# Optimization experiments

Measured on AMD Instinct MI355X. Metric: run time of the kernel, lower is better.

Reference implementation:

```python
import jax, jax.numpy as jnp
import numpy as np

B, D, H, W, C = 1, 6, 128, 128, 180
NH = 6
HD = C // NH
SCALE = HD ** -0.5
WS = (2, 8, 8)
SS = (1, 4, 4)
N = WS[0] * WS[1] * WS[2]  # 128 tokens per 3D window
HID = int(C * 2.0)  # GEGLU hidden = 360


def _rel_pos_index(ws):
    d, h, w = np.meshgrid(np.arange(ws[0]), np.arange(ws[1]), np.arange(ws[2]), indexing='ij')
    coords = np.stack([d, h, w]).reshape(3, -1)  # (3, N)
    rel = (coords[:, :, None] - coords[:, None, :]).transpose(1, 2, 0).astype(np.int64)
    rel[:, :, 0] += ws[0] - 1
    rel[:, :, 1] += ws[1] - 1
    rel[:, :, 2] += ws[2] - 1
    rel[:, :, 0] *= (2 * ws[1] - 1) * (2 * ws[2] - 1)
    rel[:, :, 1] *= (2 * ws[2] - 1)
    return rel.sum(-1).astype(np.int32)  # (N, N)


def _sine_pos(hw, nf, temperature=10000.0):
    scale = 2.0 * np.pi
    ones = np.ones((1, hw[0], hw[1]), np.float64)
    y = np.cumsum(ones, 1)
    x = np.cumsum(ones, 2)
    eps = 1e-6
    y = y / (y[:, -1:, :] + eps) * scale
    x = x / (x[:, :, -1:] + eps) * scale
    dim_t = temperature ** (2 * (np.arange(nf) // 2) / nf)
    px = x[..., None] / dim_t
    py = y[..., None] / dim_t
    px = np.stack([np.sin(px[..., 0::2]), np.cos(px[..., 1::2])], -1).reshape(1, hw[0], hw[1], -1)
    py = np.stack([np.sin(py[..., 0::2]), np.cos(py[..., 1::2])], -1).reshape(1, hw[0], hw[1], -1)
    pos = np.concatenate([py, px], -1)  # (1, H, W, 2*nf)
    return pos.reshape(1, hw[0] * hw[1], -1).astype(np.float32)


def _compute_mask():
    img = np.zeros((1, D, H, W, 1), np.float32)
    cnt = 0
    sl = lambda w, s: (slice(0, -w), slice(-w, -s), slice(-s, None))
    for ds in sl(WS[0], SS[0]):
        for hs in sl(WS[1], SS[1]):
            for ws_ in sl(WS[2], SS[2]):
                img[:, ds, hs, ws_, :] = cnt
                cnt += 1
    mw = img.reshape(1, D // WS[0], WS[0], H // WS[1], WS[1], W // WS[2], WS[2], 1)
    mw = mw.transpose(0, 1, 3, 5, 2, 4, 6, 7).reshape(-1, N)
    am = mw[:, None, :] - mw[:, :, None]
    return np.where(am != 0, -100.0, 0.0).astype(np.float32)  # (nW, N, N)


def win_part(x):
    b = x.shape[0]
    x = x.reshape(b, D // WS[0], WS[0], H // WS[1], WS[1], W // WS[2], WS[2], C)
    return x.transpose(0, 1, 3, 5, 2, 4, 6, 7).reshape(-1, N, C)


def win_rev(w, b):
    x = w.reshape(b, D // WS[0], H // WS[1], W // WS[2], WS[0], WS[1], WS[2], C)
    return x.transpose(0, 1, 4, 2, 5, 3, 6, 7).reshape(b, D, H, W, C)


def ln(x, g, b):
    m = x.mean(-1, keepdims=True)
    v = ((x - m) ** 2).mean(-1, keepdims=True)
    return (x - m) / jnp.sqrt(v + 1e-5) * g + b


def attn_fn(q, k, v, bias, mask):
    # q,k,v: (B_, NH, n, HD); bias: (NH, n, n) or None; mask: (nW, n, n) or None
    a = jnp.einsum('bhnd,bhmd->bhnm', q * SCALE, k)
    if bias is not None:
        a = a + bias[None]
    if mask is not None:
        nW = mask.shape[0]
        a = a.reshape(-1, nW, NH, a.shape[-2], a.shape[-1]) + mask[None, :, None]
        a = a.reshape(-1, NH, a.shape[-2], a.shape[-1])
    a = jax.nn.softmax(a, axis=-1)
    o = jnp.einsum('bhnm,bhmd->bhnd', a, v)
    return o.transpose(0, 2, 1, 3).reshape(o.shape[0], o.shape[2], -1)


def setup_inputs() -> dict:
    key = jax.random.key(0)
    ks = jax.random.split(key, 9)
    p = lambda k, shape: jax.random.normal(k, shape, jnp.float32) * 0.02
    return {
        'x': jax.random.normal(ks[0], (B, D, H, W, C), jnp.float32),
        'mask': jnp.asarray(_compute_mask()),
        'g1': jnp.ones((C,), jnp.float32), 'b1': jnp.zeros((C,), jnp.float32),
        'g2': jnp.ones((C,), jnp.float32), 'b2': jnp.zeros((C,), jnp.float32),
        'w_qkv_self': p(ks[1], (C, 3 * C)), 'b_qkv_self': jnp.zeros((3 * C,), jnp.float32),
        'w_qkv_mut': p(ks[2], (C, 3 * C)), 'b_qkv_mut': jnp.zeros((3 * C,), jnp.float32),
        'rpb_table': p(ks[3], ((2 * WS[0] - 1) * (2 * WS[1] - 1) * (2 * WS[2] - 1), NH)),
        'pos_bias': jnp.asarray(_sine_pos((WS[1], WS[2]), C // 2)),
        'w_proj': p(ks[4], (2 * C, C)), 'b_proj': jnp.zeros((C,), jnp.float32),
        'w_fc11': p(ks[5], (C, HID)), 'b_fc11': jnp.zeros((HID,), jnp.float32),
        'w_fc12': p(ks[6], (C, HID)), 'b_fc12': jnp.zeros((HID,), jnp.float32),
        'w_fc2': p(ks[7], (HID, C)), 'b_fc2': jnp.zeros((C,), jnp.float32),
        'rpi': jnp.asarray(_rel_pos_index(WS)),
    }


def reference(x, mask, g1, b1, g2, b2, w_qkv_self, b_qkv_self, w_qkv_mut, b_qkv_mut,
              rpb_table, pos_bias, w_proj, b_proj, w_fc11, b_fc11, w_fc12, b_fc12,
              w_fc2, b_fc2, rpi):
    # --- attention branch ---
    h = ln(x, g1, b1)
    h = jnp.roll(h, (-SS[0], -SS[1], -SS[2]), axis=(1, 2, 3))  # cyclic shift
    xw = win_part(h)  # (B*nW, N, C)
    B_ = xw.shape[0]

    def qkv(xin, wq, bq):
        t = (xin @ wq + bq).reshape(B_, -1, 3, NH, HD).transpose(2, 0, 3, 1, 4)
        return t[0], t[1], t[2]

    q, k, v = qkv(xw, w_qkv_self, b_qkv_self)
    bias = rpb_table[rpi.reshape(-1)].reshape(N, N, NH).transpose(2, 0, 1)
    x_self = attn_fn(q, k, v, bias, mask)

    # mutual attention between the two frames of each window
    pb = jnp.concatenate([pos_bias, pos_bias], axis=1)  # (1, N, C)
    qm, km, vm = qkv(xw + pb, w_qkv_mut, b_qkv_mut)
    half = N // 2
    q1, q2 = qm[:, :, :half], qm[:, :, half:]
    k1, k2 = km[:, :, :half], km[:, :, half:]
    v1, v2 = vm[:, :, :half], vm[:, :, half:]
    m2 = mask[:, :half, :half]
    x1 = attn_fn(q2, k1, v1, None, m2)
    x2 = attn_fn(q1, k2, v2, None, m2)
    xo = jnp.concatenate([jnp.concatenate([x1, x2], axis=1), x_self], axis=2)  # (B_, N, 2C)
    xo = xo @ w_proj + b_proj
    out = win_rev(xo, x.shape[0])
    out = jnp.roll(out, (SS[0], SS[1], SS[2]), axis=(1, 2, 3))
    x = x + out

    # --- GEGLU MLP branch ---
    h = ln(x, g2, b2)
    h = jax.nn.gelu(h @ w_fc11 + b_fc11, approximate=False) * (h @ w_fc12 + b_fc12)
    x = x + (h @ w_fc2 + b_fc2)
    return x
```

## Files before the change

### kernel.cpp

```cpp
#include <hip/hip_runtime.h>
#include <hip/hip_bf16.h>
#include <math.h>
#include <cstdio>


typedef __hip_bfloat16 bf16;
typedef __attribute__((ext_vector_type(8))) short short8;
typedef __attribute__((ext_vector_type(4))) unsigned short us4;
typedef __attribute__((ext_vector_type(4))) float f32x4;

#define SCALE_F 0.18257418583505536f
#define SZPE 18874368u

__device__ __forceinline__ bf16  f2b(float v){ return __float2bfloat16(v); }
__device__ __forceinline__ float bu2f(unsigned short u){
    union { unsigned int i; float f; } x; x.i = ((unsigned int)u) << 16; return x.f;
}
__device__ __forceinline__ f32x4 mfma16(short8 a, short8 b, f32x4 c){
    return __builtin_amdgcn_mfma_f32_16x16x32_bf16(a, b, c, 0, 0, 0);
}

__device__ __forceinline__ void gld16(const bf16* g, bf16* s){
    __builtin_amdgcn_global_load_lds(
        (const __attribute__((address_space(1))) unsigned int*)g,
        (__attribute__((address_space(3))) unsigned int*)s, 16, 0, 0);
}

__device__ __forceinline__ float gelu_erf(float x){
    float z  = fabsf(x) * 0.70710678118654752f;
    float t  = __builtin_amdgcn_rcpf(fmaf(0.3275911f, z, 1.f));
    float p  = fmaf(fmaf(fmaf(fmaf(1.061405429f, t, -1.453152027f),
                              t, 1.421413741f), t, -0.284496736f), t, 0.254829592f) * t;
    float e  = __expf(-z * z);
    float er = fmaf(-p, e, 1.f);
    er = (x >= 0.f) ? er : -er;
    return 0.5f * x * (1.f + er);
}

__device__ __forceinline__ int xswz(){
    return (blockIdx.x & 7) * ((int)gridDim.x >> 3) + ((int)blockIdx.x >> 3);
}

__device__ __forceinline__ int wincnt(int win, int tok){
    int d = (win >> 8) * 2 + (tok >> 6);
    int h = ((win >> 4) & 15) * 8 + ((tok >> 3) & 7);
    int w = (win & 15) * 8 + (tok & 7);
    int rd = (d >= 4) + (d >= 5);
    int rh = (h >= 120) + (h >= 124);
    int rw = (w >= 120) + (w >= 124);
    return (rd * 3 + rh) * 3 + rw;
}

__device__ __forceinline__ size_t wrev_base(int row){
    int win = row >> 7, tok = row & 127;
    int wd = win >> 8, wh = (win >> 4) & 15, ww = win & 15;
    int td = tok >> 6, th = (tok >> 3) & 7, tw = tok & 7;
    int d = wd * 2 + td + 1; if (d >= 6) d -= 6;
    int h = (wh * 8 + th + 4) & 127;
    int wcol = (ww * 8 + tw + 4) & 127;
    return ((size_t)((d * 128 + h) * 128 + wcol)) * 180;
}

__global__ __launch_bounds__(256) void k_pack_qkv(const float* __restrict__ w,
                                                  const float* __restrict__ bias,
                                                  bf16* __restrict__ Bt,
                                                  float* __restrict__ bb)
{
    int idx = blockIdx.x * 256 + threadIdx.x;
    int n = idx / 192, k = idx - n * 192;
    int three = n / 192;
    int rem = n - three * 192, nh = rem >> 5, hdp = rem & 31;
    int srcc = three * 180 + nh * 30 + hdp;
    float v = 0.f;
    if (hdp < 30 && k < 180) v = w[(size_t)k * 540 + srcc];
    if (three == 0) v *= SCALE_F;
    Bt[(size_t)n * 192 + k] = f2b(v);
    if (k == 0) bb[n] = (hdp < 30) ? ((three == 0 ? SCALE_F : 1.f) * bias[srcc]) : 0.f;
}

__global__ __launch_bounds__(256) void k_pack(const float* __restrict__ w,
                                              int NW, int K, int KP,
                                              bf16* __restrict__ Bt)
{
    int idx = blockIdx.x * 256 + threadIdx.x;
    int n = idx / KP, k = idx - n * KP;
    float v = (n < NW && k < K) ? w[(size_t)k * NW + n] : 0.f;
    Bt[idx] = f2b(v);
}

__global__ __launch_bounds__(256) void k_rpbg(const float* __restrict__ rpb,
                                              const int* __restrict__ rpi,
                                              bf16* __restrict__ biasrT)
{
    int n = blockIdx.x * 256 + threadIdx.x;
    int nh = n >> 14, rc = n & 16383;
    int row = rc >> 7, col = rc & 127;
    biasrT[((size_t)nh * 128 + col) * 128 + row] = f2b(rpb[rpi[rc] * 6 + nh]);
}

__global__ __launch_bounds__(256) void k_zpad(bf16* __restrict__ attn)
{
    int gi = blockIdx.x * 256 + threadIdx.x;
    int row = gi / 3, part = gi - row * 3;
    *(uint4*)&attn[(size_t)row * 384 + 360 + part * 8] = make_uint4(0u,0u,0u,0u);
}

template<bool ROLL_PB>
__global__ __launch_bounds__(256) void k_ln(const float* __restrict__ x,
                                            const float* __restrict__ g,
                                            const float* __restrict__ b,
                                            const float* __restrict__ pb,
                                            bf16* __restrict__ xw,
                                            bf16* __restrict__ xwm)
{
    int row  = blockIdx.x * 4 + (threadIdx.x >> 6);
    int lane = threadIdx.x & 63;
    const float* src;
    if (ROLL_PB) {
        src = x + wrev_base(row) - 0;
    } else {
        src = x + (size_t)row * 180;
    }
    float v0 = src[lane];
    float v1 = src[lane + 64];
    float v2 = (lane < 52) ? src[lane + 128] : 0.f;
    float s  = v0 + v1 + v2;
    float ss = v0*v0 + v1*v1 + v2*v2;
    #pragma unroll
    for (int o = 32; o > 0; o >>= 1) { s += __shfl_xor(s, o, 64); ss += __shfl_xor(ss, o, 64); }
    float mean = s * (1.f/180.f);
    float var  = ss * (1.f/180.f) - mean*mean;
    float rstd = rsqrtf(var + 1e-5f);

    bf16* dst = xw + (size_t)row * 192;
    float y0 = (v0-mean)*rstd*g[lane]     + b[lane];
    float y1 = (v1-mean)*rstd*g[lane+64]  + b[lane+64];
    float y2 = (lane < 52) ? ((v2-mean)*rstd*g[lane+128] + b[lane+128]) : 0.f;
    dst[lane]      = f2b(y0);
    dst[lane+64]   = f2b(y1);
    if (lane < 52) dst[lane+128] = f2b(y2);
    if (lane < 12) dst[180+lane] = f2b(0.f);
    if (ROLL_PB) {
        const float* pbr = pb + (size_t)(row & 63) * 180;
        bf16* dm = xwm + (size_t)row * 192;
        dm[lane]      = f2b(y0 + pbr[lane]);
        dm[lane+64]   = f2b(y1 + pbr[lane+64]);
        if (lane < 52) dm[lane+128] = f2b(y2 + pbr[lane+128]);
        if (lane < 12) dm[180+lane] = f2b(0.f);
    }
}

template<int KP, bool DUAL>
__device__ __forceinline__ void mm2(const bf16* __restrict__ A,
                                    const bf16* __restrict__ Bt1,
                                    const bf16* __restrict__ Bt2,
                                    bf16* As, bf16* Bs1, bf16* Bs2,
                                    int m0, int n0,
                                    f32x4 (&acc1)[2][4], f32x4 (&acc2)[2][4])
{
    const int tid = threadIdx.x;
    const int w = tid >> 6, l = tid & 63, q = l >> 4, c = l & 15;
    const int lr = l >> 3, lj = l & 7;
    const int swz = ((lj ^ lr) << 3);
    #pragma unroll
    for (int ks = 0; ks < KP / 64; ks++) {
        #pragma unroll
        for (int e = 0; e < 4; e++) {
            int m = (e * 4 + w) * 8 + lr;
            gld16(&A[(size_t)(m0 + m) * KP + ks * 64 + swz], &As[((e * 4 + w) * 8) * 64]);
        }
        #pragma unroll
        for (int e = 0; e < 2; e++) {
            int n = (e * 4 + w) * 8 + lr;
            gld16(&Bt1[(size_t)(n0 + n) * KP + ks * 64 + swz], &Bs1[((e * 4 + w) * 8) * 64]);
            if (DUAL)
                gld16(&Bt2[(size_t)(n0 + n) * KP + ks * 64 + swz], &Bs2[((e * 4 + w) * 8) * 64]);
        }
        __syncthreads();
        #pragma unroll
        for (int k32 = 0; k32 < 2; k32++) {
            int koff = (((k32 * 4 + q) ^ (c & 7)) << 3);
            short8 a[2];
            #pragma unroll
            for (int mt = 0; mt < 2; mt++)
                a[mt] = *(const short8*)&As[(w * 32 + mt * 16 + c) * 64 + koff];
            #pragma unroll
            for (int nt = 0; nt < 4; nt++) {
                short8 b1 = *(const short8*)&Bs1[(nt * 16 + c) * 64 + koff];
                #pragma unroll
                for (int mt = 0; mt < 2; mt++) acc1[mt][nt] = mfma16(a[mt], b1, acc1[mt][nt]);
                if (DUAL) {
                    short8 b2 = *(const short8*)&Bs2[(nt * 16 + c) * 64 + koff];
                    #pragma unroll
                    for (int mt = 0; mt < 2; mt++) acc2[mt][nt] = mfma16(a[mt], b2, acc2[mt][nt]);
                }
            }
        }
        __syncthreads();
    }
}

__device__ __forceinline__ int cs_idx(int row, int colt){
    return row * 64 + ((((colt >> 3) ^ ((row >> 2) & 7)) << 3) | (colt & 7));
}

__global__ __launch_bounds__(256) void k_qkv(const bf16* __restrict__ A,
                                             const bf16* __restrict__ Bt,
                                             const float* __restrict__ bb,
                                             bf16* __restrict__ outq)
{
    __shared__ __align__(16) bf16 As[128 * 64];
    __shared__ __align__(16) bf16 Bs[64 * 64];
    int bid = xswz();
    int n0 = (bid % 9) * 64, m0 = (bid / 9) * 128;
    f32x4 a1[2][4] = {}, a2[2][4];
    mm2<192, false>(A, Bt, nullptr, As, Bs, nullptr, m0, n0, a1, a2);

    int tid = threadIdx.x, w = tid >> 6, l = tid & 63, q = l >> 4, c = l & 15;
    bf16* Cs = As;
    #pragma unroll
    for (int mt = 0; mt < 2; mt++)
      #pragma unroll
      for (int nt = 0; nt < 4; nt++)
        #pragma unroll
        for (int r = 0; r < 4; r++) {
            int row = w * 32 + mt * 16 + q * 4 + r;
            int colt = nt * 16 + c;
            Cs[cs_idx(row, colt)] = f2b(a1[mt][nt][r] + bb[n0 + colt]);
        }
    __syncthreads();
    int win = m0 >> 7;
    #pragma unroll
    for (int e = 0; e < 4; e++) {
        int gi = e * 256 + tid;
        int row = gi >> 3, j = gi & 7, c8 = j * 8;
        int col = n0 + c8;
        int three = col / 192, rem = col - three * 192;
        int nh = rem >> 5, hdp = rem & 31;
        bf16* dst = outq + (size_t)three * SZPE + ((size_t)(win * 6 + nh) * 128 + row) * 32 + hdp;
        *(uint4*)dst = *(const uint4*)&Cs[row * 64 + ((j ^ ((row >> 2) & 7)) << 3)];
    }
}

__global__ __launch_bounds__(256) void k_proj(const bf16* __restrict__ A,
                                              const bf16* __restrict__ Bt,
                                              const float* __restrict__ bias,
                                              const float* __restrict__ xin,
                                              float* __restrict__ res)
{
    __shared__ __align__(16) char smem[24576];
    bf16*  As = (bf16*)smem;
    bf16*  Bs = (bf16*)(smem + 16384);
    float* Cs = (float*)smem;
    int bid = xswz();
    int n0 = (bid % 3) * 64, m0 = (bid / 3) * 128;
    f32x4 a1[2][4] = {}, a2[2][4];
    mm2<384, false>(A, Bt, nullptr, As, Bs, nullptr, m0, n0, a1, a2);

    int tid = threadIdx.x, w = tid >> 6, l = tid & 63, q = l >> 4, c = l & 15;
    #pragma unroll
    for (int h = 0; h < 2; h++) {
        __syncthreads();
        if ((w >> 1) == h) {
            #pragma unroll
            for (int mt = 0; mt < 2; mt++)
              #pragma unroll
              for (int nt = 0; nt < 4; nt++)
                #pragma unroll
                for (int r = 0; r < 4; r++) {
                    int rl = (w & 1) * 32 + mt * 16 + q * 4 + r;
                    Cs[rl * 76 + nt * 16 + c] = a1[mt][nt][r];
                }
        }
        __syncthreads();
        #pragma unroll
        for (int e = 0; e < 4; e++) {
            int slot = e * 256 + tid;
            int rl = slot >> 4, cq = slot & 15;
            int col = n0 + cq * 4;
            if (col < 180) {
                size_t base = wrev_base(m0 + h * 64 + rl) + col;
                float4 xi = *(const float4*)&xin[base];
                float4 bi = *(const float4*)&bias[col];
                const float* cp = &Cs[rl * 76 + cq * 4];
                float4 o;
                o.x = xi.x + cp[0] + bi.x;
                o.y = xi.y + cp[1] + bi.y;
                o.z = xi.z + cp[2] + bi.z;
                o.w = xi.w + cp[3] + bi.w;
                *(float4*)&res[base] = o;
            }
        }
    }
}

__global__ __launch_bounds__(256) void k_fc1(const bf16* __restrict__ A,
                                             const bf16* __restrict__ Bt1,
                                             const float* __restrict__ bb1,
                                             const bf16* __restrict__ Bt2,
                                             const float* __restrict__ bb2,
                                             bf16* __restrict__ hid)
{
    __shared__ __align__(16) bf16 As[128 * 64];
    __shared__ __align__(16) bf16 Bs1[64 * 64];
    __shared__ __align__(16) bf16 Bs2[64 * 64];
    int bid = xswz();
    int n0 = (bid % 6) * 64, m0 = (bid / 6) * 128;
    f32x4 a1[2][4] = {}, a2[2][4] = {};
    mm2<192, true>(A, Bt1, Bt2, As, Bs1, Bs2, m0, n0, a1, a2);

    int tid = threadIdx.x, w = tid >> 6, l = tid & 63, q = l >> 4, c = l & 15;
    bf16* Cs = As;
    #pragma unroll
    for (int mt = 0; mt < 2; mt++)
      #pragma unroll
      for (int nt = 0; nt < 4; nt++)
        #pragma unroll
        for (int r = 0; r < 4; r++) {
            int row = w * 32 + mt * 16 + q * 4 + r;
            int colt = nt * 16 + c;
            int col = n0 + colt;
            float hv = 0.f;
            if (col < 360)
                hv = gelu_erf(a1[mt][nt][r] + bb1[col]) * (a2[mt][nt][r] + bb2[col]);
            Cs[cs_idx(row, colt)] = f2b(hv);
        }
    __syncthreads();
    #pragma unroll
    for (int e = 0; e < 4; e++) {
        int gi = e * 256 + tid;
        int row = gi >> 3, j = gi & 7, c8 = j * 8;
        *(uint4*)&hid[(size_t)(m0 + row) * 384 + n0 + c8] =
            *(const uint4*)&Cs[row * 64 + ((j ^ ((row >> 2) & 7)) << 3)];
    }
}

__global__ __launch_bounds__(256) void k_fc2(const bf16* __restrict__ A,
                                             const bf16* __restrict__ Bt,
                                             const float* __restrict__ bias,
                                             float* __restrict__ out)
{
    __shared__ __align__(16) char smem[24576];
    bf16*  As = (bf16*)smem;
    bf16*  Bs = (bf16*)(smem + 16384);
    float* Cs = (float*)smem;
    int bid = xswz();
    int n0 = (bid % 3) * 64, m0 = (bid / 3) * 128;
    f32x4 a1[2][4] = {}, a2[2][4];
    mm2<384, false>(A, Bt, nullptr, As, Bs, nullptr, m0, n0, a1, a2);

    int tid = threadIdx.x, w = tid >> 6, l = tid & 63, q = l >> 4, c = l & 15;
    #pragma unroll
    for (int h = 0; h < 2; h++) {
        __syncthreads();
        if ((w >> 1) == h) {
            #pragma unroll
            for (int mt = 0; mt < 2; mt++)
              #pragma unroll
              for (int nt = 0; nt < 4; nt++)
                #pragma unroll
                for (int r = 0; r < 4; r++) {
                    int rl = (w & 1) * 32 + mt * 16 + q * 4 + r;
                    Cs[rl * 76 + nt * 16 + c] = a1[mt][nt][r];
                }
        }
        __syncthreads();
        #pragma unroll
        for (int e = 0; e < 4; e++) {
            int slot = e * 256 + tid;
            int rl = slot >> 4, cq = slot & 15;
            int col = n0 + cq * 4;
            if (col < 180) {
                size_t idx = (size_t)(m0 + h * 64 + rl) * 180 + col;
                float4 ov = *(const float4*)&out[idx];
                float4 bi = *(const float4*)&bias[col];
                const float* cp = &Cs[rl * 76 + cq * 4];
                ov.x += cp[0] + bi.x;
                ov.y += cp[1] + bi.y;
                ov.z += cp[2] + bi.z;
                ov.w += cp[3] + bi.w;
                *(float4*)&out[idx] = ov;
            }
        }
    }
}

template<bool MUT>
__global__ __launch_bounds__(256) void k_attn(const bf16* __restrict__ qkv,
                                              const bf16* __restrict__ biasrT,
                                              bf16* __restrict__ aout)
{
    __shared__ __align__(16) bf16 Vts[32 * 136];
    __shared__ __align__(16) bf16 Ps[128 * 136];

    int wh = blockIdx.x, win = wh / 6, nh = wh - win * 6;
    const bf16* qg = qkv + (size_t)wh * 4096;
    const bf16* kg = qg + (size_t)SZPE;
    const bf16* vg = qg + 2 * (size_t)SZPE;
    int tid = threadIdx.x, w = tid >> 6, l = tid & 63, q = l >> 4, c = l & 15;

    #pragma unroll
    for (int e = 0; e < 2; e++) {
        int base = (e * 256 + tid) * 8;
        int tok = base >> 5, hd0 = base & 31;
        uint4 vv = *(const uint4*)&vg[base];
        const bf16* pv = (const bf16*)&vv;
        #pragma unroll
        for (int i = 0; i < 8; i++) {
            int hd = hd0 + i;
            Vts[hd * 136 + (tok ^ (((hd >> 3) & 3) << 3))] = pv[i];
        }
    }

    f32x4 S[2][8];
    #pragma unroll
    for (int mt = 0; mt < 2; mt++)
        #pragma unroll
        for (int nt = 0; nt < 8; nt++) S[mt][nt] = (f32x4){0.f, 0.f, 0.f, 0.f};
    {
        short8 a[2];
        #pragma unroll
        for (int mt = 0; mt < 2; mt++) {
            int rq = w * 32 + mt * 16 + c;
            if (MUT) rq ^= 64;
            a[mt] = *(const short8*)&qg[rq * 32 + q * 8];
        }
        #pragma unroll
        for (int nt = 0; nt < 8; nt++) {
            short8 b = *(const short8*)&kg[(nt * 16 + c) * 32 + q * 8];
            #pragma unroll
            for (int mt = 0; mt < 2; mt++) S[mt][nt] = mfma16(a[mt], b, S[mt][nt]);
        }
    }

    int rcnt[2][4], ccnt[8];
    #pragma unroll
    for (int mt = 0; mt < 2; mt++)
        #pragma unroll
        for (int r = 0; r < 4; r++) {
            int row = w * 32 + mt * 16 + q * 4 + r;
            rcnt[mt][r] = wincnt(win, MUT ? (row & 63) : row);
        }
    #pragma unroll
    for (int nt = 0; nt < 8; nt++) {
        int col = nt * 16 + c;
        ccnt[nt] = wincnt(win, MUT ? (col & 63) : col);
    }

    float mx[2][4];
    #pragma unroll
    for (int mt = 0; mt < 2; mt++)
      #pragma unroll
      for (int r = 0; r < 4; r++) mx[mt][r] = -3.0e38f;

    #pragma unroll
    for (int mt = 0; mt < 2; mt++)
      #pragma unroll
      for (int nt = 0; nt < 8; nt++) {
        float bv[4];
        if (!MUT) {
            int col = nt * 16 + c;
            us4 bb = *(const us4*)&biasrT[((size_t)(nh * 128 + col)) * 128
                                          + w * 32 + mt * 16 + q * 4];
            #pragma unroll
            for (int r = 0; r < 4; r++) bv[r] = bu2f(bb[r]);
        }
        bool valid = (w < 2) == (nt < 4);
        #pragma unroll
        for (int r = 0; r < 4; r++) {
            float s = S[mt][nt][r];
            if (MUT) {
                s = (rcnt[mt][r] == ccnt[nt]) ? s : s - 100.f;
                s = valid ? s : -30000.f;
            } else {
                s += bv[r];
                if (rcnt[mt][r] != ccnt[nt]) s -= 100.f;
            }
            S[mt][nt][r] = s;
            mx[mt][r] = fmaxf(mx[mt][r], s);
        }
      }
    #pragma unroll
    for (int mt = 0; mt < 2; mt++)
      #pragma unroll
      for (int r = 0; r < 4; r++) {
          float m = mx[mt][r];
          #pragma unroll
          for (int o = 1; o < 16; o <<= 1) m = fmaxf(m, __shfl_xor(m, o, 64));
          mx[mt][r] = m;
      }

    float sm[2][4] = {};
    #pragma unroll
    for (int mt = 0; mt < 2; mt++)
      #pragma unroll
      for (int nt = 0; nt < 8; nt++)
        #pragma unroll
        for (int r = 0; r < 4; r++) {
            float p = __expf(S[mt][nt][r] - mx[mt][r]);
            sm[mt][r] += p;
            Ps[(w * 32 + mt * 16 + q * 4 + r) * 136 + ((nt * 16 + c) ^ (q << 3))] = f2b(p);
        }
    #pragma unroll
    for (int mt = 0; mt < 2; mt++)
      #pragma unroll
      for (int r = 0; r < 4; r++) {
          float s = sm[mt][r];
          #pragma unroll
          for (int o = 1; o < 16; o <<= 1) s += __shfl_xor(s, o, 64);
          sm[mt][r] = s;
      }
    __syncthreads();

    f32x4 O[2][2];
    #pragma unroll
    for (int mt = 0; mt < 2; mt++)
        #pragma unroll
        for (int nt = 0; nt < 2; nt++) O[mt][nt] = (f32x4){0.f, 0.f, 0.f, 0.f};
    #pragma unroll
    for (int ks = 0; ks < 4; ks++) {
        short8 a[2];
        #pragma unroll
        for (int mt = 0; mt < 2; mt++) {
            int row = w * 32 + mt * 16 + c;
            int xr = ((c >> 2) & 3) << 3;
            a[mt] = *(const short8*)&Ps[row * 136 + (ks * 32 + ((q << 3) ^ xr))];
        }
        #pragma unroll
        for (int nt = 0; nt < 2; nt++) {
            int hd = nt * 16 + c;
            int xv = ((hd >> 3) & 3) << 3;
            short8 b = *(const short8*)&Vts[hd * 136 + (ks * 32 + ((q << 3) ^ xv))];
            #pragma unroll
            for (int mt = 0; mt < 2; mt++) O[mt][nt] = mfma16(a[mt], b, O[mt][nt]);
        }
    }

    #pragma unroll
    for (int mt = 0; mt < 2; mt++)
      #pragma unroll
      for (int r = 0; r < 4; r++) {
          int row = w * 32 + mt * 16 + q * 4 + r;
          float inv = 1.f / sm[mt][r];
          #pragma unroll
          for (int nt = 0; nt < 2; nt++) {
              int col = nt * 16 + c;
              if (col < 30)
                  aout[((size_t)win * 128 + row) * 384 + (MUT ? 0 : 180) + nh * 30 + col] =
                      f2b(O[mt][nt][r] * inv);
          }
      }
}

extern "C" void kernel_launch(void* const* d_in, const int* in_sizes, int n_in,
                              void* d_out, int out_size, void* d_ws, size_t ws_size,
                              hipStream_t stream)
{
    const float* x     = (const float*)d_in[0];
    const float* mask  = (const float*)d_in[1];
    const float* g1    = (const float*)d_in[2];
    const float* b1    = (const float*)d_in[3];
    const float* g2    = (const float*)d_in[4];
    const float* b2    = (const float*)d_in[5];
    const float* wqs   = (const float*)d_in[6];
    const float* bqs   = (const float*)d_in[7];
    const float* wqm   = (const float*)d_in[8];
    const float* bqm   = (const float*)d_in[9];
    const float* rpb   = (const float*)d_in[10];
    const float* posb  = (const float*)d_in[11];
    const float* wproj = (const float*)d_in[12];
    const float* bproj = (const float*)d_in[13];
    const float* w11   = (const float*)d_in[14];
    const float* bf11  = (const float*)d_in[15];
    const float* w12   = (const float*)d_in[16];
    const float* bf12  = (const float*)d_in[17];
    const float* w2    = (const float*)d_in[18];
    const float* bf2   = (const float*)d_in[19];
    const int*   rpi   = (const int*)d_in[20];
    float* out = (float*)d_out;
    (void)mask;

    const size_t need = 265671168;
    if (ws_size < need) { fprintf(stderr, "[tmsa] ws too small: %zu < %zu\n", ws_size, need); return; }

    char* W = (char*)d_ws;
    bf16*  xw     = (bf16*)W;
    bf16*  xwm    = (bf16*)(W + 37748736);
    bf16*  attn   = (bf16*)(W + 75497472);
    bf16*  qkv    = (bf16*)(W + 150994944);
    bf16*  biasrT = (bf16*)(W + 264241152);
    bf16*  Btqs   = (bf16*)(W + 264634368);
    bf16*  Btqm   = (bf16*)(W + 264855552);
    float* bbqs   = (float*)(W + 265076736);
    float* bbqm   = (float*)(W + 265079040);
    bf16*  Btproj = (bf16*)(W + 265081344);
    bf16*  Btf11  = (bf16*)(W + 265228800);
    bf16*  Btf12  = (bf16*)(W + 265376256);
    bf16*  Btf2   = (bf16*)(W + 265523712);

    k_rpbg<<<dim3(384), 256, 0, stream>>>(rpb, rpi, biasrT);
    k_pack_qkv<<<dim3(432), 256, 0, stream>>>(wqs, bqs, Btqs, bbqs);
    k_pack_qkv<<<dim3(432), 256, 0, stream>>>(wqm, bqm, Btqm, bbqm);
    k_pack<<<dim3(288), 256, 0, stream>>>(wproj, 180, 360, 384, Btproj);
    k_pack<<<dim3(288), 256, 0, stream>>>(w11,   360, 180, 192, Btf11);
    k_pack<<<dim3(288), 256, 0, stream>>>(w12,   360, 180, 192, Btf12);
    k_pack<<<dim3(288), 256, 0, stream>>>(w2,    180, 360, 384, Btf2);

    k_ln<true><<<dim3(24576), 256, 0, stream>>>(x, g1, b1, posb, xw, xwm);
    k_zpad<<<dim3(1152), 256, 0, stream>>>(attn);
    k_qkv<<<dim3(6912), 256, 0, stream>>>(xw, Btqs, bbqs, qkv);
    k_attn<false><<<dim3(4608), 256, 0, stream>>>(qkv, biasrT, attn);
    k_qkv<<<dim3(6912), 256, 0, stream>>>(xwm, Btqm, bbqm, qkv);
    k_attn<true><<<dim3(4608), 256, 0, stream>>>(qkv, biasrT, attn);
    k_proj<<<dim3(2304), 256, 0, stream>>>(attn, Btproj, bproj, x, out);
    k_ln<false><<<dim3(24576), 256, 0, stream>>>(out, g2, b2, nullptr, xw, nullptr);
    k_fc1<<<dim3(4608), 256, 0, stream>>>(xw, Btf11, bf11, Btf12, bf12, attn);
    k_fc2<<<dim3(2304), 256, 0, stream>>>(attn, Btf2, bf2, out);
}
```

Measured before the change: 590.9 us.

## Merge setup kernels, vectorize layernorm, skip masked half in mutual attention

Seven weight-pack and bias-gather kernels plus the zero-pad kernel are merged into a single k_prep launch that dispatches on block index, cutting launch overhead. Layernorm now uses float4 loads and packed 4-wide bf16 stores instead of scalar accesses. Mutual attention computes only the 64 valid key columns per wave instead of all 128 with -30000 masking, halving its QK, softmax and PV work. These are three unrelated edits, and the block-index ranges in k_prep must exactly match the old grid sizes.

```diff
diff --git a/kernel.cpp b/kernel.cpp
--- a/kernel.cpp
+++ b/kernel.cpp
@@ -15,6 +15,13 @@
 __device__ __forceinline__ bf16  f2b(float v){ return __float2bfloat16(v); }
 __device__ __forceinline__ float bu2f(unsigned short u){
     union { unsigned int i; float f; } x; x.i = ((unsigned int)u) << 16; return x.f;
+}
+__device__ __forceinline__ us4 pack4(float a, float b, float c, float d){
+    us4 r;
+    bf16 t0 = f2b(a), t1 = f2b(b), t2 = f2b(c), t3 = f2b(d);
+    r[0] = *(unsigned short*)&t0; r[1] = *(unsigned short*)&t1;
+    r[2] = *(unsigned short*)&t2; r[3] = *(unsigned short*)&t3;
+    return r;
 }
 __device__ __forceinline__ f32x4 mfma16(short8 a, short8 b, f32x4 c){
     return __builtin_amdgcn_mfma_f32_16x16x32_bf16(a, b, c, 0, 0, 0);
@@ -61,12 +68,9 @@
     return ((size_t)((d * 128 + h) * 128 + wcol)) * 180;
 }
 
-__global__ __launch_bounds__(256) void k_pack_qkv(const float* __restrict__ w,
-                                                  const float* __restrict__ bias,
-                                                  bf16* __restrict__ Bt,
-                                                  float* __restrict__ bb)
-{
-    int idx = blockIdx.x * 256 + threadIdx.x;
+__device__ __forceinline__ void prep_pack_qkv(int idx, const float* w, const float* bias,
+                                              bf16* Bt, float* bb)
+{
     int n = idx / 192, k = idx - n * 192;
     int three = n / 192;
     int rem = n - three * 192, nh = rem >> 5, hdp = rem & 31;
@@ -77,32 +81,57 @@
     Bt[(size_t)n * 192 + k] = f2b(v);
     if (k == 0) bb[n] = (hdp < 30) ? ((three == 0 ? SCALE_F : 1.f) * bias[srcc]) : 0.f;
 }
-
-__global__ __launch_bounds__(256) void k_pack(const float* __restrict__ w,
-                                              int NW, int K, int KP,
-                                              bf16* __restrict__ Bt)
-{
-    int idx = blockIdx.x * 256 + threadIdx.x;
+__device__ __forceinline__ void prep_pack(int idx, const float* w,
+                                          int NW, int K, int KP, bf16* Bt)
+{
     int n = idx / KP, k = idx - n * KP;
     float v = (n < NW && k < K) ? w[(size_t)k * NW + n] : 0.f;
     Bt[idx] = f2b(v);
 }
-
-__global__ __launch_bounds__(256) void k_rpbg(const float* __restrict__ rpb,
+__global__ __launch_bounds__(256) void k_prep(const float* __restrict__ rpb,
                                               const int* __restrict__ rpi,
-                                              bf16* __restrict__ biasrT)
-{
-    int n = blockIdx.x * 256 + threadIdx.x;
-    int nh = n >> 14, rc = n & 16383;
-    int row = rc >> 7, col = rc & 127;
-    biasrT[((size_t)nh * 128 + col) * 128 + row] = f2b(rpb[rpi[rc] * 6 + nh]);
-}
-
-__global__ __launch_bounds__(256) void k_zpad(bf16* __restrict__ attn)
-{
-    int gi = blockIdx.x * 256 + threadIdx.x;
-    int row = gi / 3, part = gi - row * 3;
-    *(uint4*)&attn[(size_t)row * 384 + 360 + part * 8] = make_uint4(0u,0u,0u,0u);
+                                              bf16* __restrict__ biasrT,
+                                              const float* __restrict__ wqs,
+                                              const float* __restrict__ bqs,
+                                              bf16* __restrict__ Btqs,
+                                              float* __restrict__ bbqs,
+                                              const float* __restrict__ wqm,
+                                              const float* __restrict__ bqm,
+                                              bf16* __restrict__ Btqm,
+                                              float* __restrict__ bbqm,
+                                              const float* __restrict__ wproj,
+                                              bf16* __restrict__ Btproj,
+                                              const float* __restrict__ w11,
+                                              bf16* __restrict__ Btf11,
+                                              const float* __restrict__ w12,
+                                              bf16* __restrict__ Btf12,
+                                              const float* __restrict__ w2,
+                                              bf16* __restrict__ Btf2,
+                                              bf16* __restrict__ attn)
+{
+    int bid = blockIdx.x, tid = threadIdx.x;
+    if (bid < 384) {
+        int n = bid * 256 + tid;
+        int nh = n >> 14, rc = n & 16383;
+        int row = rc >> 7, col = rc & 127;
+        biasrT[((size_t)nh * 128 + col) * 128 + row] = f2b(rpb[rpi[rc] * 6 + nh]);
+    } else if (bid < 816) {
+        prep_pack_qkv((bid - 384) * 256 + tid, wqs, bqs, Btqs, bbqs);
+    } else if (bid < 1248) {
+        prep_pack_qkv((bid - 816) * 256 + tid, wqm, bqm, Btqm, bbqm);
+    } else if (bid < 1536) {
+        prep_pack((bid - 1248) * 256 + tid, wproj, 180, 360, 384, Btproj);
+    } else if (bid < 1824) {
+        prep_pack((bid - 1536) * 256 + tid, w11, 360, 180, 192, Btf11);
+    } else if (bid < 2112) {
+        prep_pack((bid - 1824) * 256 + tid, w12, 360, 180, 192, Btf12);
+    } else if (bid < 2400) {
+        prep_pack((bid - 2112) * 256 + tid, w2, 180, 360, 384, Btf2);
+    } else {
+        int gi = (bid - 2400) * 256 + tid;
+        int row = gi / 3, part = gi - row * 3;
+        *(uint4*)&attn[(size_t)row * 384 + 360 + part * 8] = make_uint4(0u,0u,0u,0u);
+    }
 }
 
 template<bool ROLL_PB>
@@ -115,17 +144,11 @@
 {
     int row  = blockIdx.x * 4 + (threadIdx.x >> 6);
     int lane = threadIdx.x & 63;
-    const float* src;
-    if (ROLL_PB) {
-        src = x + wrev_base(row) - 0;
-    } else {
-        src = x + (size_t)row * 180;
-    }
-    float v0 = src[lane];
-    float v1 = src[lane + 64];
-    float v2 = (lane < 52) ? src[lane + 128] : 0.f;
-    float s  = v0 + v1 + v2;
-    float ss = v0*v0 + v1*v1 + v2*v2;
+    const float* src = ROLL_PB ? (x + wrev_base(row)) : (x + (size_t)row * 180);
+    float4 v = make_float4(0.f, 0.f, 0.f, 0.f);
+    if (lane < 45) v = *(const float4*)&src[lane * 4];
+    float s  = v.x + v.y + v.z + v.w;
+    float ss = v.x*v.x + v.y*v.y + v.z*v.z + v.w*v.w;
     #pragma unroll
     for (int o = 32; o > 0; o >>= 1) { s += __shfl_xor(s, o, 64); ss += __shfl_xor(ss, o, 64); }
     float mean = s * (1.f/180.f);
@@ -133,20 +156,27 @@
     float rstd = rsqrtf(var + 1e-5f);
 
     bf16* dst = xw + (size_t)row * 192;
-    float y0 = (v0-mean)*rstd*g[lane]     + b[lane];
-    float y1 = (v1-mean)*rstd*g[lane+64]  + b[lane+64];
-    float y2 = (lane < 52) ? ((v2-mean)*rstd*g[lane+128] + b[lane+128]) : 0.f;
-    dst[lane]      = f2b(y0);
-    dst[lane+64]   = f2b(y1);
-    if (lane < 52) dst[lane+128] = f2b(y2);
-    if (lane < 12) dst[180+lane] = f2b(0.f);
+    float4 y = make_float4(0.f, 0.f, 0.f, 0.f);
+    if (lane < 45) {
+        float4 gv = *(const float4*)&g[lane * 4];
+        float4 bv = *(const float4*)&b[lane * 4];
+        y.x = (v.x - mean) * rstd * gv.x + bv.x;
+        y.y = (v.y - mean) * rstd * gv.y + bv.y;
+        y.z = (v.z - mean) * rstd * gv.z + bv.z;
+        y.w = (v.w - mean) * rstd * gv.w + bv.w;
+        *(us4*)&dst[lane * 4] = pack4(y.x, y.y, y.z, y.w);
+    } else if (lane < 48) {
+        *(us4*)&dst[lane * 4] = (us4){0, 0, 0, 0};
+    }
     if (ROLL_PB) {
-        const float* pbr = pb + (size_t)(row & 63) * 180;
         bf16* dm = xwm + (size_t)row * 192;
-        dm[lane]      = f2b(y0 + pbr[lane]);
-        dm[lane+64]   = f2b(y1 + pbr[lane+64]);
-        if (lane < 52) dm[lane+128] = f2b(y2 + pbr[lane+128]);
-        if (lane < 12) dm[180+lane] = f2b(0.f);
+        if (lane < 45) {
+            const float* pbr = pb + (size_t)(row & 63) * 180;
+            float4 pv = *(const float4*)&pbr[lane * 4];
+            *(us4*)&dm[lane * 4] = pack4(y.x + pv.x, y.y + pv.y, y.z + pv.z, y.w + pv.w);
+        } else if (lane < 48) {
+            *(us4*)&dm[lane * 4] = (us4){0, 0, 0, 0};
+        }
     }
 }
 
@@ -399,6 +429,9 @@
     const bf16* vg = qg + 2 * (size_t)SZPE;
     int tid = threadIdx.x, w = tid >> 6, l = tid & 63, q = l >> 4, c = l & 15;
 
+    constexpr int NT = MUT ? 4 : 8;
+    const int colbase = MUT ? ((w < 2) ? 0 : 64) : 0;
+
     #pragma unroll
     for (int e = 0; e < 2; e++) {
         int base = (e * 256 + tid) * 8;
@@ -412,11 +445,11 @@
         }
     }
 
-    f32x4 S[2][8];
-    #pragma unroll
-    for (int mt = 0; mt < 2; mt++)
-        #pragma unroll
-        for (int nt = 0; nt < 8; nt++) S[mt][nt] = (f32x4){0.f, 0.f, 0.f, 0.f};
+    f32x4 S[2][NT];
+    #pragma unroll
+    for (int mt = 0; mt < 2; mt++)
+        #pragma unroll
+        for (int nt = 0; nt < NT; nt++) S[mt][nt] = (f32x4){0.f, 0.f, 0.f, 0.f};
     {
         short8 a[2];
         #pragma unroll
@@ -426,14 +459,14 @@
             a[mt] = *(const short8*)&qg[rq * 32 + q * 8];
         }
         #pragma unroll
-        for (int nt = 0; nt < 8; nt++) {
-            short8 b = *(const short8*)&kg[(nt * 16 + c) * 32 + q * 8];
+        for (int nt = 0; nt < NT; nt++) {
+            short8 b = *(const short8*)&kg[(colbase + nt * 16 + c) * 32 + q * 8];
             #pragma unroll
             for (int mt = 0; mt < 2; mt++) S[mt][nt] = mfma16(a[mt], b, S[mt][nt]);
         }
     }
 
-    int rcnt[2][4], ccnt[8];
+    int rcnt[2][4], ccnt[NT];
     #pragma unroll
     for (int mt = 0; mt < 2; mt++)
         #pragma unroll
@@ -442,8 +475,8 @@
             rcnt[mt][r] = wincnt(win, MUT ? (row & 63) : row);
         }
     #pragma unroll
-    for (int nt = 0; nt < 8; nt++) {
-        int col = nt * 16 + c;
+    for (int nt = 0; nt < NT; nt++) {
+        int col = colbase + nt * 16 + c;
         ccnt[nt] = wincnt(win, MUT ? (col & 63) : col);
     }
 
@@ -456,7 +489,7 @@
     #pragma unroll
     for (int mt = 0; mt < 2; mt++)
       #pragma unroll
-      for (int nt = 0; nt < 8; nt++) {
+      for (int nt = 0; nt < NT; nt++) {
         float bv[4];
         if (!MUT) {
             int col = nt * 16 + c;
@@ -465,13 +498,11 @@
             #pragma unroll
             for (int r = 0; r < 4; r++) bv[r] = bu2f(bb[r]);
         }
-        bool valid = (w < 2) == (nt < 4);
         #pragma unroll
         for (int r = 0; r < 4; r++) {
             float s = S[mt][nt][r];
             if (MUT) {
                 s = (rcnt[mt][r] == ccnt[nt]) ? s : s - 100.f;
-                s = valid ? s : -30000.f;
             } else {
                 s += bv[r];
                 if (rcnt[mt][r] != ccnt[nt]) s -= 100.f;
@@ -494,12 +525,12 @@
     #pragma unroll
     for (int mt = 0; mt < 2; mt++)
       #pragma unroll
-      for (int nt = 0; nt < 8; nt++)
+      for (int nt = 0; nt < NT; nt++)
         #pragma unroll
         for (int r = 0; r < 4; r++) {
             float p = __expf(S[mt][nt][r] - mx[mt][r]);
             sm[mt][r] += p;
-            Ps[(w * 32 + mt * 16 + q * 4 + r) * 136 + ((nt * 16 + c) ^ (q << 3))] = f2b(p);
+            Ps[(w * 32 + mt * 16 + q * 4 + r) * 136 + ((colbase + nt * 16 + c) ^ (q << 3))] = f2b(p);
         }
     #pragma unroll
     for (int mt = 0; mt < 2; mt++)
@@ -518,7 +549,8 @@
         #pragma unroll
         for (int nt = 0; nt < 2; nt++) O[mt][nt] = (f32x4){0.f, 0.f, 0.f, 0.f};
     #pragma unroll
-    for (int ks = 0; ks < 4; ks++) {
+    for (int ksr = 0; ksr < (MUT ? 2 : 4); ksr++) {
+        int ks = MUT ? ((colbase >> 5) + ksr) : ksr;
         short8 a[2];
         #pragma unroll
         for (int mt = 0; mt < 2; mt++) {
@@ -598,16 +630,13 @@
     bf16*  Btf12  = (bf16*)(W + 265376256);
     bf16*  Btf2   = (bf16*)(W + 265523712);
 
-    k_rpbg<<<dim3(384), 256, 0, stream>>>(rpb, rpi, biasrT);
-    k_pack_qkv<<<dim3(432), 256, 0, stream>>>(wqs, bqs, Btqs, bbqs);
-    k_pack_qkv<<<dim3(432), 256, 0, stream>>>(wqm, bqm, Btqm, bbqm);
-    k_pack<<<dim3(288), 256, 0, stream>>>(wproj, 180, 360, 384, Btproj);
-    k_pack<<<dim3(288), 256, 0, stream>>>(w11,   360, 180, 192, Btf11);
-    k_pack<<<dim3(288), 256, 0, stream>>>(w12,   360, 180, 192, Btf12);
-    k_pack<<<dim3(288), 256, 0, stream>>>(w2,    180, 360, 384, Btf2);
+    k_prep<<<dim3(3552), 256, 0, stream>>>(rpb, rpi, biasrT,
+                                           wqs, bqs, Btqs, bbqs,
+                                           wqm, bqm, Btqm, bbqm,
+                                           wproj, Btproj, w11, Btf11,
+                                           w12, Btf12, w2, Btf2, attn);
 
     k_ln<true><<<dim3(24576), 256, 0, stream>>>(x, g1, b1, posb, xw, xwm);
-    k_zpad<<<dim3(1152), 256, 0, stream>>>(attn);
     k_qkv<<<dim3(6912), 256, 0, stream>>>(xw, Btqs, bbqs, qkv);
     k_attn<false><<<dim3(4608), 256, 0, stream>>>(qkv, biasrT, attn);
     k_qkv<<<dim3(6912), 256, 0, stream>>>(xwm, Btqm, bbqm, qkv);
```

After: 580.6 us. Within noise of the previous version (-1.7%).
